# Optimization experiments

Hardware: AMD Instinct MI355X
Metric: run time of the kernel (lower is better)

The kernel has to match this reference:

```python
import jax, jax.numpy as jnp
import numpy as np

N = 11616          # IMDB total nodes (hard-coded slices in source)
NHID = 512
L = 4              # num_layers (encoder and decoder each)
E = 371712         # ~32 avg degree
SIZES = [4278, 2081, 5257]
FEATS = [3066, 2081, 5257]
GAMMA = 3.0


def setup_inputs() -> dict:
    key = jax.random.key(0)
    ks = jax.random.split(key, 24)
    s = 0.02
    d = {}
    d["X0"] = jax.random.normal(ks[0], (SIZES[0], FEATS[0]), jnp.float32)
    d["X1"] = jax.random.normal(ks[1], (SIZES[1], FEATS[1]), jnp.float32)
    d["X2"] = jax.random.normal(ks[2], (SIZES[2], FEATS[2]), jnp.float32)
    d["src"] = jax.random.randint(ks[3], (E,), 0, N)
    d["dst"] = jax.random.randint(ks[4], (E,), 0, N)
    d["edge_w"] = jax.random.uniform(ks[5], (E,), jnp.float32) / 32.0  # ~normalized adjacency values
    d["adj_full"] = (jax.random.uniform(ks[6], (N, N), jnp.float32) < 0.005).astype(jnp.float32)
    # input projections fc_list: feat_dim -> nhid
    for i in range(3):
        d[f"fc_W{i}"] = jax.random.normal(ks[7 + i], (FEATS[i], NHID), jnp.float32) * s
        d[f"fc_b{i}"] = jnp.zeros((NHID,), jnp.float32)
    # stacked GraphConvolution weights (encoder / decoder)
    d["enc_W"] = jax.random.normal(ks[10], (L, NHID, NHID), jnp.float32) * s
    d["enc_b"] = jnp.zeros((L, NHID), jnp.float32)
    d["dec_W"] = jax.random.normal(ks[11], (L, NHID, NHID), jnp.float32) * s
    d["dec_b"] = jnp.zeros((L, NHID), jnp.float32)
    # output projections fc_list2: nhid -> feat_dim
    for i in range(3):
        d[f"out_W{i}"] = jax.random.normal(ks[12 + i], (NHID, FEATS[i]), jnp.float32) * s
        d[f"out_b{i}"] = jnp.zeros((FEATS[i],), jnp.float32)
    return d


def reference(X0, X1, X2, edge_w, adj_full,
              fc_W0, fc_b0, fc_W1, fc_b1, fc_W2, fc_b2,
              enc_W, enc_b, dec_W, dec_b,
              out_W0, out_b0, out_W1, out_b1, out_W2, out_b2,
              src, dst):
    def spmm(h):  # sparse A @ h via edge list
        return jax.ops.segment_sum(h[src] * edge_w[:, None], dst, num_segments=N)

    # per-type input projection, concat over node types -> [N, NHID]
    x = jnp.concatenate([X0 @ fc_W0 + fc_b0,
                         X1 @ fc_W1 + fc_b1,
                         X2 @ fc_W2 + fc_b2], axis=0)

    # encoder then decoder; per source: relu+dropout only at layer 0 (L>1 branch),
    # residual add for layers i>0; dropout is identity in eval mode.
    for W, b in ((enc_W, enc_b), (dec_W, dec_b)):
        for i in range(L):
            h = spmm(x @ W[i]) + b[i]
            x = jax.nn.relu(h) if i == 0 else x + h

    # IMDB slices of final embedding
    e0, e1, e2 = x[:SIZES[0]], x[SIZES[0]:SIZES[0] + SIZES[1]], x[SIZES[0] + SIZES[1]:]
    r0 = e0 @ out_W0 + out_b0
    r1 = e1 @ out_W1 + out_b1
    r2 = e2 @ out_W2 + out_b2

    # emb_loss_fun2: BCE(sigmoid(x x^T), adj_full), mean. Stable form:
    z = x @ x.T  # [N, N]
    emb_loss = jnp.mean(adj_full * jax.nn.softplus(-z) + (1.0 - adj_full) * jax.nn.softplus(z))

    # recon_loss_fun2 on type-0 features (cosine-based, power gamma)
    rn = r0 / jnp.maximum(jnp.linalg.norm(r0, axis=-1, keepdims=True), 1e-12)
    fn = X0 / jnp.maximum(jnp.linalg.norm(X0, axis=1, keepdims=True), 1e-12)
    recon_loss = jnp.mean((1.0 - jnp.sum(rn * fn, axis=-1)) ** GAMMA)

    return (r0, r1, r2, emb_loss, recon_loss)
```

## Files before the change

### kernel.cpp

```cpp
#include <hip/hip_runtime.h>
#include <math.h>

#define N_NODES 11616
#define NROWPAD 11776
#define NHID    512
#define EDGES   371712
#define S0 4278
#define S1 2081
#define S2 5257
#define F0 3066
#define F1 2081
#define F2 5257
#define NBLK 91
#define NZBLK 4186
#define FC_KS 4
#define WPR 363

typedef __attribute__((ext_vector_type(8))) short bf16x8;
typedef __attribute__((ext_vector_type(4))) float f32x4;

#define GL2LDS(g, l) __builtin_amdgcn_global_load_lds(                         \
    (const __attribute__((address_space(1))) unsigned int*)(g),                \
    (__attribute__((address_space(3))) unsigned int*)(l), 16, 0, 0)

__device__ __forceinline__ int slot_of(int row, int kg)
{
    return row * 4 + (kg ^ ((row >> 1) & 3));
}

__device__ __forceinline__ float bf2f(short s)
{
    return __uint_as_float(((unsigned)(unsigned short)s) << 16);
}

__global__ void k_init(double* __restrict__ accum, int* __restrict__ indeg,
                       int* __restrict__ cursor)
{
    int i = blockIdx.x * blockDim.x + threadIdx.x;
    if (i < 2) accum[i] = 0.0;
    if (i < N_NODES) { indeg[i] = 0; cursor[i] = 0; }
}

__global__ void k_padzero(short* __restrict__ xh, short* __restrict__ xl)
{
    int i = blockIdx.x * blockDim.x + threadIdx.x;
    const int base  = N_NODES * NHID;
    const int total = (NROWPAD - N_NODES) * NHID;
    if (i < total) { xh[base + i] = 0; xl[base + i] = 0; }
}

__global__ void k_adjbits(const float* __restrict__ adj, unsigned* __restrict__ bits)
{
    const long i = (long)blockIdx.x * 256 + threadIdx.x;
    const long total = (long)N_NODES * WPR;
    if (i >= total) return;
    const int r = (int)(i / WPR);
    const int w = (int)(i % WPR);
    const float4* rp = reinterpret_cast<const float4*>(adj + (long)r * N_NODES + w * 32);
    unsigned m = 0;
    #pragma unroll
    for (int j4 = 0; j4 < 8; ++j4) {
        float4 v = rp[j4];
        int b = j4 * 4;
        m |= (v.x != 0.f) ? (1u << b)       : 0u;
        m |= (v.y != 0.f) ? (1u << (b + 1)) : 0u;
        m |= (v.z != 0.f) ? (1u << (b + 2)) : 0u;
        m |= (v.w != 0.f) ? (1u << (b + 3)) : 0u;
    }
    bits[i] = m;
}

__global__ void k_count(const int* __restrict__ dst, int* __restrict__ indeg)
{
    int e = blockIdx.x * blockDim.x + threadIdx.x;
    if (e < EDGES) atomicAdd(&indeg[dst[e]], 1);
}

__global__ void k_scan(const int* __restrict__ indeg, int* __restrict__ rowptr)
{
    __shared__ int part[256];
    const int t = threadIdx.x;
    const int chunk = (N_NODES + 255) / 256;
    const int base = t * chunk;
    int s = 0;
    for (int i = 0; i < chunk; ++i) {
        int idx = base + i;
        if (idx < N_NODES) s += indeg[idx];
    }
    part[t] = s;
    __syncthreads();
    if (t == 0) for (int i = 1; i < 256; ++i) part[i] += part[i - 1];
    __syncthreads();
    int run = (t == 0) ? 0 : part[t - 1];
    for (int i = 0; i < chunk; ++i) {
        int idx = base + i;
        if (idx < N_NODES) { rowptr[idx] = run; run += indeg[idx]; }
    }
    if (t == 0) rowptr[N_NODES] = part[255];
}

__global__ void k_fill(const int* __restrict__ src, const int* __restrict__ dst,
                       const float* __restrict__ ew, const int* __restrict__ rowptr,
                       int* __restrict__ cursor, int* __restrict__ csrc,
                       float* __restrict__ cw)
{
    int e = blockIdx.x * blockDim.x + threadIdx.x;
    if (e >= EDGES) return;
    int d = dst[e];
    int pos = rowptr[d] + atomicAdd(&cursor[d], 1);
    csrc[pos] = src[e];
    cw[pos]   = ew[e];
}

__device__ __forceinline__ void split_bf16(float f, short& hi, short& lo)
{
    unsigned u  = __float_as_uint(f);
    unsigned hr = (u + 0x7FFFu + ((u >> 16) & 1u)) & 0xFFFF0000u;
    float    fh = __uint_as_float(hr);
    float    fl = f - fh;
    unsigned ul = __float_as_uint(fl);
    unsigned lr = ul + 0x7FFFu + ((ul >> 16) & 1u);
    hi = (short)(hr >> 16);
    lo = (short)(lr >> 16);
}

__global__ void k_splitpad(const float* __restrict__ in, short* __restrict__ oh,
                           short* __restrict__ ol, int R, int C, int Cpad)
{
    const int c = blockIdx.x * 256 + threadIdx.x;
    const int r = blockIdx.y;
    if (c >= Cpad) return;
    float f = (r < R && c < C) ? in[(long)r * C + c] : 0.f;
    short h, l;
    split_bf16(f, h, l);
    oh[(long)r * Cpad + c] = h;
    ol[(long)r * Cpad + c] = l;
}

__global__ void k_tsplit(const float* __restrict__ in, short* __restrict__ oh,
                         short* __restrict__ ol, int R, int C, int Rpad, int Cpad)
{
    __shared__ float tile[32][33];
    const int cb = blockIdx.x * 32, rb = blockIdx.y * 32;
    const int tx = threadIdx.x, ty = threadIdx.y;
    #pragma unroll
    for (int i = ty; i < 32; i += 8) {
        int r = rb + i, c = cb + tx;
        tile[i][tx] = (r < R && c < C) ? in[(long)r * C + c] : 0.f;
    }
    __syncthreads();
    #pragma unroll
    for (int i = ty; i < 32; i += 8) {
        int row = cb + i, col = rb + tx;
        if (row < Cpad && col < Rpad) {
            short h, l;
            split_bf16(tile[tx][i], h, l);
            oh[(long)row * Rpad + col] = h;
            ol[(long)row * Rpad + col] = l;
        }
    }
}

__device__ __forceinline__ void stage_gl(const short* __restrict__ src, int ldk,
                                         int k0, short* ldsPanel, int lane)
{
    #pragma unroll
    for (int i = 0; i < 8; ++i) {
        int ci  = i * 64 + lane;
        int row = ci >> 2;
        int kgs = (ci & 3) ^ ((row >> 1) & 3);
        const short* g = src + (long)row * ldk + k0 + kgs * 8;
        GL2LDS(g, (char*)ldsPanel + i * 1024);
    }
}

__global__ __launch_bounds__(256, 3)
void k_gemm_bb(const short* __restrict__ Agh, const short* __restrict__ Agl,
               const short* __restrict__ Bgh, const short* __restrict__ Bgl,
               const float* __restrict__ bias, float* __restrict__ C,
               int M, int NN, int Kpad, int ldk)
{
    __shared__ short P[4][4096];
    const int t = threadIdx.x, lane = t & 63, w = t >> 6;
    const int rowBase = blockIdx.y * 128, colBase = blockIdx.x * 128;
    const int wm = (w >> 1) * 64, wn = (w & 1) * 64;
    const int kg = lane >> 4, fr = lane & 15;

    const short* srcs[4] = { Agh + (long)rowBase * ldk, Agl + (long)rowBase * ldk,
                             Bgh + (long)colBase * ldk, Bgl + (long)colBase * ldk };
    const short* mySrc = srcs[w];

    int offA[4], offB[4];
    #pragma unroll
    for (int f = 0; f < 4; ++f) {
        int rA = wm + f * 16 + fr, rB = wn + f * 16 + fr;
        offA[f] = slot_of(rA, kg) * 8;
        offB[f] = slot_of(rB, kg) * 8;
    }

    f32x4 acc[4][4];
    #pragma unroll
    for (int i = 0; i < 4; ++i)
        #pragma unroll
        for (int j = 0; j < 4; ++j)
            acc[i][j] = (f32x4){0.f, 0.f, 0.f, 0.f};

    for (int k0 = 0; k0 < Kpad; k0 += 32) {
        stage_gl(mySrc, ldk, k0, &P[w][0], lane);
        __syncthreads();
        bf16x8 ah[4], al[4], bh[4], bl[4];
        #pragma unroll
        for (int f = 0; f < 4; ++f) {
            ah[f] = *(const bf16x8*)&P[0][offA[f]];
            al[f] = *(const bf16x8*)&P[1][offA[f]];
            bh[f] = *(const bf16x8*)&P[2][offB[f]];
            bl[f] = *(const bf16x8*)&P[3][offB[f]];
        }
        #pragma unroll
        for (int i = 0; i < 4; ++i)
            #pragma unroll
            for (int j = 0; j < 4; ++j) {
                acc[i][j] = __builtin_amdgcn_mfma_f32_16x16x32_bf16(ah[i], bh[j], acc[i][j], 0, 0, 0);
                acc[i][j] = __builtin_amdgcn_mfma_f32_16x16x32_bf16(ah[i], bl[j], acc[i][j], 0, 0, 0);
                acc[i][j] = __builtin_amdgcn_mfma_f32_16x16x32_bf16(al[i], bh[j], acc[i][j], 0, 0, 0);
            }
        __syncthreads();
    }

    #pragma unroll
    for (int i = 0; i < 4; ++i) {
        #pragma unroll
        for (int q = 0; q < 4; ++q) {
            int r = rowBase + wm + i * 16 + kg * 4 + q;
            if (r >= M) continue;
            #pragma unroll
            for (int j = 0; j < 4; ++j) {
                int c = colBase + wn + j * 16 + fr;
                if (c < NN)
                    C[(long)r * NN + c] = acc[i][j][q] + (bias ? bias[c] : 0.f);
            }
        }
    }
}

__global__ __launch_bounds__(256, 3)
void k_gemm_red(const short* __restrict__ Agh, const short* __restrict__ Agl,
                const short* __restrict__ Bgh, const short* __restrict__ Bgl,
                float* __restrict__ Cpart, int M, int ldk, int kChunk)
{
    __shared__ short P[4][4096];
    const int t = threadIdx.x, lane = t & 63, w = t >> 6;
    const int rowBase = blockIdx.y * 128, colBase = blockIdx.x * 128;
    const int z = blockIdx.z;
    const int wm = (w >> 1) * 64, wn = (w & 1) * 64;
    const int kg = lane >> 4, fr = lane & 15;

    const short* srcs[4] = { Agh + (long)rowBase * ldk, Agl + (long)rowBase * ldk,
                             Bgh + (long)colBase * ldk, Bgl + (long)colBase * ldk };
    const short* mySrc = srcs[w];

    int offA[4], offB[4];
    #pragma unroll
    for (int f = 0; f < 4; ++f) {
        int rA = wm + f * 16 + fr, rB = wn + f * 16 + fr;
        offA[f] = slot_of(rA, kg) * 8;
        offB[f] = slot_of(rB, kg) * 8;
    }

    f32x4 acc[4][4];
    #pragma unroll
    for (int i = 0; i < 4; ++i)
        #pragma unroll
        for (int j = 0; j < 4; ++j)
            acc[i][j] = (f32x4){0.f, 0.f, 0.f, 0.f};

    const int kEnd = z * kChunk + kChunk;
    for (int k0 = z * kChunk; k0 < kEnd; k0 += 32) {
        stage_gl(mySrc, ldk, k0, &P[w][0], lane);
        __syncthreads();
        bf16x8 ah[4], al[4], bh[4], bl[4];
        #pragma unroll
        for (int f = 0; f < 4; ++f) {
            ah[f] = *(const bf16x8*)&P[0][offA[f]];
            al[f] = *(const bf16x8*)&P[1][offA[f]];
            bh[f] = *(const bf16x8*)&P[2][offB[f]];
            bl[f] = *(const bf16x8*)&P[3][offB[f]];
        }
        #pragma unroll
        for (int i = 0; i < 4; ++i)
            #pragma unroll
            for (int j = 0; j < 4; ++j) {
                acc[i][j] = __builtin_amdgcn_mfma_f32_16x16x32_bf16(ah[i], bh[j], acc[i][j], 0, 0, 0);
                acc[i][j] = __builtin_amdgcn_mfma_f32_16x16x32_bf16(ah[i], bl[j], acc[i][j], 0, 0, 0);
                acc[i][j] = __builtin_amdgcn_mfma_f32_16x16x32_bf16(al[i], bh[j], acc[i][j], 0, 0, 0);
            }
        __syncthreads();
    }

    #pragma unroll
    for (int i = 0; i < 4; ++i) {
        #pragma unroll
        for (int q = 0; q < 4; ++q) {
            int r = rowBase + wm + i * 16 + kg * 4 + q;
            if (r >= M) continue;
            #pragma unroll
            for (int j = 0; j < 4; ++j) {
                int c = colBase + wn + j * 16 + fr;
                Cpart[((long)z * M + r) * NHID + c] = acc[i][j][q];
            }
        }
    }
}

__global__ void k_fcreduce(const float* __restrict__ Cpart, const float* __restrict__ bias,
                           int M, short* __restrict__ oh, short* __restrict__ ol)
{
    const int r = blockIdx.x;
    const int c = threadIdx.x << 2;
    float4 s = *reinterpret_cast<const float4*>(bias + c);
    #pragma unroll
    for (int z = 0; z < FC_KS; ++z) {
        const float4 p = *reinterpret_cast<const float4*>(Cpart + ((long)z * M + r) * NHID + c);
        s.x += p.x; s.y += p.y; s.z += p.z; s.w += p.w;
    }
    short4 h, l;
    split_bf16(s.x, h.x, l.x); split_bf16(s.y, h.y, l.y);
    split_bf16(s.z, h.z, l.z); split_bf16(s.w, h.w, l.w);
    *reinterpret_cast<short4*>(oh + (long)r * NHID + c) = h;
    *reinterpret_cast<short4*>(ol + (long)r * NHID + c) = l;
}

__global__ __launch_bounds__(256, 3)
void k_zloss(const short* __restrict__ xh, const short* __restrict__ xl,
             const unsigned* __restrict__ bits, double* __restrict__ accum)
{
    __shared__ short P[4][4096];
    __shared__ float ztr[4][16][17];
    __shared__ float red[256];
    const int t = threadIdx.x, lane = t & 63, w = t >> 6;

    int L;
    {
        const int q = NZBLK / 8, rr = NZBLK % 8;
        int d = blockIdx.x;
        int xcd = d & 7, pos = d >> 3;
        L = (xcd < rr) ? xcd * (q + 1) + pos : rr * (q + 1) + (xcd - rr) * q + pos;
    }
    int R, Cb;
    {
        int RS = 0;
        for (;;) {
            int nr  = min(4, NBLK - RS * 4);
            int tri = nr * (nr + 1) / 2;
            int rest = NBLK - (RS + 1) * 4;
            if (rest < 0) rest = 0;
            int band = tri + nr * rest;
            if (L < band) break;
            L -= band; ++RS;
        }
        int nr  = min(4, NBLK - RS * 4);
        int tri = nr * (nr + 1) / 2;
        if (L < tri) {
            int r = 0;
            while (L >= nr - r) { L -= nr - r; ++r; }
            R  = RS * 4 + r;
            Cb = RS * 4 + r + L;
        } else {
            L -= tri;
            int CS = RS + 1;
            for (;;) {
                int nc  = min(4, NBLK - CS * 4);
                int cnt = nr * nc;
                if (L < cnt) { R = RS * 4 + L / nc; Cb = CS * 4 + L % nc; break; }
                L -= cnt; ++CS;
            }
        }
    }
    const int rowBase = R * 128, colBase = Cb * 128;
    const int diag = (Cb == R);

    const int wm = (w >> 1) * 64, wn = (w & 1) * 64;
    const int kg = lane >> 4, fr = lane & 15;

    const short* srcs[4] = { xh + (long)rowBase * NHID, xl + (long)rowBase * NHID,
                             xh + (long)colBase * NHID, xl + (long)colBase * NHID };
    const short* mySrc = srcs[w];

    int offA[4], offB[4];
    #pragma unroll
    for (int f = 0; f < 4; ++f) {
        int rA = wm + f * 16 + fr, rB = wn + f * 16 + fr;
        offA[f] = slot_of(rA, kg) * 8;
        offB[f] = slot_of(rB, kg) * 8;
    }

    f32x4 acc[4][4];
    #pragma unroll
    for (int i = 0; i < 4; ++i)
        #pragma unroll
        for (int j = 0; j < 4; ++j)
            acc[i][j] = (f32x4){0.f, 0.f, 0.f, 0.f};

    for (int k0 = 0; k0 < NHID; k0 += 32) {
        stage_gl(mySrc, NHID, k0, &P[w][0], lane);
        __syncthreads();
        bf16x8 ah[4], al[4], bh[4], bl[4];
        #pragma unroll
        for (int f = 0; f < 4; ++f) {
            ah[f] = *(const bf16x8*)&P[0][offA[f]];
            al[f] = *(const bf16x8*)&P[1][offA[f]];
            bh[f] = *(const bf16x8*)&P[2][offB[f]];
            bl[f] = *(const bf16x8*)&P[3][offB[f]];
        }
        #pragma unroll
        for (int i = 0; i < 4; ++i)
            #pragma unroll
            for (int j = 0; j < 4; ++j) {
                acc[i][j] = __builtin_amdgcn_mfma_f32_16x16x32_bf16(ah[i], bh[j], acc[i][j], 0, 0, 0);
                acc[i][j] = __builtin_amdgcn_mfma_f32_16x16x32_bf16(ah[i], bl[j], acc[i][j], 0, 0, 0);
                acc[i][j] = __builtin_amdgcn_mfma_f32_16x16x32_bf16(al[i], bh[j], acc[i][j], 0, 0, 0);
            }
        __syncthreads();
    }

    float local = 0.f;
    #pragma unroll
    for (int i = 0; i < 4; ++i) {
        #pragma unroll
        for (int q = 0; q < 4; ++q) {
            int r = rowBase + wm + i * 16 + kg * 4 + q;
            if (r >= N_NODES) continue;
            #pragma unroll
            for (int j = 0; j < 4; ++j) {
                int c = colBase + wn + j * 16 + fr;
                if (c >= N_NODES) continue;
                float z  = acc[i][j][q];
                float sp = fmaxf(z, 0.f) + __logf(1.f + __expf(-fabsf(z)));
                unsigned wd = bits[(long)r * WPR + (c >> 5)];
                float az = ((wd >> (c & 31)) & 1u) ? z : 0.f;
                local += diag ? (sp - az) : (2.f * sp - az);
            }
        }
    }
    if (!diag) {
        #pragma unroll
        for (int i = 0; i < 4; ++i) {
            #pragma unroll
            for (int j = 0; j < 4; ++j) {
                #pragma unroll
                for (int q = 0; q < 4; ++q)
                    ztr[w][kg * 4 + q][fr] = acc[i][j][q];
                #pragma unroll
                for (int q = 0; q < 4; ++q) {
                    float zt = ztr[w][fr][kg * 4 + q];
                    int cc = colBase + wn + j * 16 + kg * 4 + q;
                    int rr = rowBase + wm + i * 16 + fr;
                    if (cc < N_NODES && rr < N_NODES) {
                        unsigned wd = bits[(long)cc * WPR + (rr >> 5)];
                        if ((wd >> (rr & 31)) & 1u) local -= zt;
                    }
                }
            }
        }
    }
    red[t] = local;
    __syncthreads();
    for (int sft = 128; sft > 0; sft >>= 1) {
        if (t < sft) red[t] += red[t + sft];
        __syncthreads();
    }
    if (t == 0) atomicAdd(accum, (double)red[0]);
}

__global__ void k_spmm(const float* __restrict__ y,
                       const int* __restrict__ rowptr, const int* __restrict__ csrc,
                       const float* __restrict__ cw, const float* __restrict__ bias,
                       int do_relu, short* __restrict__ xh, short* __restrict__ xl)
{
    const int wv   = threadIdx.x >> 6;
    const int lane = threadIdx.x & 63;
    const int n    = blockIdx.x * 2 + (wv >> 1);
    const int c    = (wv & 1) * 256 + (lane << 2);
    float4 s = make_float4(0.f, 0.f, 0.f, 0.f);
    const int beg = rowptr[n], end = rowptr[n + 1];
    for (int e = beg; e < end; ++e) {
        int   sn = csrc[e];
        float wt = cw[e];
        const float4 yv = *reinterpret_cast<const float4*>(y + (long)sn * NHID + c);
        s.x = fmaf(wt, yv.x, s.x);
        s.y = fmaf(wt, yv.y, s.y);
        s.z = fmaf(wt, yv.z, s.z);
        s.w = fmaf(wt, yv.w, s.w);
    }
    const float4 bv = *reinterpret_cast<const float4*>(bias + c);
    float4 o;
    o.x = s.x + bv.x; o.y = s.y + bv.y; o.z = s.z + bv.z; o.w = s.w + bv.w;
    if (do_relu) {
        o.x = fmaxf(o.x, 0.f); o.y = fmaxf(o.y, 0.f);
        o.z = fmaxf(o.z, 0.f); o.w = fmaxf(o.w, 0.f);
    } else {
        const short4 h4 = *reinterpret_cast<const short4*>(xh + (long)n * NHID + c);
        const short4 l4 = *reinterpret_cast<const short4*>(xl + (long)n * NHID + c);
        o.x += bf2f(h4.x) + bf2f(l4.x);
        o.y += bf2f(h4.y) + bf2f(l4.y);
        o.z += bf2f(h4.z) + bf2f(l4.z);
        o.w += bf2f(h4.w) + bf2f(l4.w);
    }
    short4 h, l;
    split_bf16(o.x, h.x, l.x); split_bf16(o.y, h.y, l.y);
    split_bf16(o.z, h.z, l.z); split_bf16(o.w, h.w, l.w);
    *reinterpret_cast<short4*>(xh + (long)n * NHID + c) = h;
    *reinterpret_cast<short4*>(xl + (long)n * NHID + c) = l;
}

__global__ void k_recon(const float* __restrict__ r0, const float* __restrict__ X0,
                        double* __restrict__ accum)
{
    const int row = blockIdx.x;
    const int t = threadIdx.x;
    float dot = 0.f, nr = 0.f, nf = 0.f;
    for (int c = t; c < F0; c += 256) {
        float a = r0[(long)row * F0 + c];
        float b = X0[(long)row * F0 + c];
        dot = fmaf(a, b, dot);
        nr  = fmaf(a, a, nr);
        nf  = fmaf(b, b, nf);
    }
    #pragma unroll
    for (int o = 32; o > 0; o >>= 1) {
        dot += __shfl_down(dot, o);
        nr  += __shfl_down(nr, o);
        nf  += __shfl_down(nf, o);
    }
    __shared__ float sd[3][4];
    const int lane = t & 63, wid = t >> 6;
    if (lane == 0) { sd[0][wid] = dot; sd[1][wid] = nr; sd[2][wid] = nf; }
    __syncthreads();
    if (t == 0) {
        float d = sd[0][0] + sd[0][1] + sd[0][2] + sd[0][3];
        float a = sd[1][0] + sd[1][1] + sd[1][2] + sd[1][3];
        float b = sd[2][0] + sd[2][1] + sd[2][2] + sd[2][3];
        float cosv = d / (fmaxf(sqrtf(a), 1e-12f) * fmaxf(sqrtf(b), 1e-12f));
        float v = 1.f - cosv;
        atomicAdd(accum + 1, (double)(v * v * v));
    }
}

__global__ void k_final(const double* __restrict__ accum, float* __restrict__ out)
{
    if (threadIdx.x == 0) {
        out[45082958] = (float)(accum[0] / ((double)N_NODES * (double)N_NODES));
        out[45082959] = (float)(accum[1] / (double)S0);
    }
}

extern "C" void kernel_launch(void* const* d_in, const int* in_sizes, int n_in,
                              void* d_out, int out_size, void* d_ws, size_t ws_size,
                              hipStream_t stream)
{
    const float* X0  = (const float*)d_in[0];
    const float* X1  = (const float*)d_in[1];
    const float* X2  = (const float*)d_in[2];
    const int*   src = (const int*)d_in[3];
    const int*   dst = (const int*)d_in[4];
    const float* ew  = (const float*)d_in[5];
    const float* adj = (const float*)d_in[6];
    const float* fcW[3]  = {(const float*)d_in[7],  (const float*)d_in[9],  (const float*)d_in[11]};
    const float* fcB[3]  = {(const float*)d_in[8],  (const float*)d_in[10], (const float*)d_in[12]};
    const float* encW = (const float*)d_in[13];
    const float* encB = (const float*)d_in[14];
    const float* decW = (const float*)d_in[15];
    const float* decB = (const float*)d_in[16];
    const float* outW[3] = {(const float*)d_in[17], (const float*)d_in[19], (const float*)d_in[21]};
    const float* outB[3] = {(const float*)d_in[18], (const float*)d_in[20], (const float*)d_in[22]};
    float* out = (float*)d_out;

    const int FD[3]     = {F0, F1, F2};
    const int FPAD[3]   = {(F0 + 127) & ~127, (F1 + 127) & ~127, (F2 + 127) & ~127};
    const int SPAD[3]   = {(S0 + 127) & ~127, (S1 + 127) & ~127, (S2 + 127) & ~127};
    const int SD[3]     = {S0, S1, S2};
    const float* XD[3]  = {X0, X1, X2};

    char* ws = (char*)d_ws;
    size_t off = 0;
    auto alloc = [&](size_t bytes) { void* p = ws + off; off += (bytes + 255) & ~(size_t)255; return p; };

    double* accum = (double*)alloc(16);
    const size_t XB = (size_t)N_NODES * NHID * sizeof(float);
    float* ybuf = (float*)alloc(XB);
    float* xalt = (float*)alloc(XB);
    short* xh   = (short*)alloc((size_t)NROWPAD * NHID * 2);
    short* xl   = (short*)alloc((size_t)NROWPAD * NHID * 2);
    const size_t XSmax = (size_t)5376 * 5376;
    short* Xsh  = (short*)alloc(XSmax * 2);
    short* Xsl  = (short*)alloc(XSmax * 2);
    short* fcWh = (short*)alloc((size_t)NHID * 5376 * 2);
    short* fcWl = (short*)alloc((size_t)NHID * 5376 * 2);
    short* wTh  = (short*)alloc((size_t)8 * NHID * NHID * 2);
    short* wTl  = (short*)alloc((size_t)8 * NHID * NHID * 2);
    unsigned* bits = (unsigned*)alloc((size_t)N_NODES * WPR * 4);
    int* indeg  = (int*)alloc((size_t)N_NODES * 4);
    int* rowptr = (int*)alloc((size_t)(N_NODES + 1) * 4);
    int* cursor = (int*)alloc((size_t)N_NODES * 4);
    int* csrc   = (int*)alloc((size_t)EDGES * 4);
    float* cw   = (float*)alloc((size_t)EDGES * 4);

    float* cpart = ybuf;

    k_init<<<dim3((N_NODES + 255) / 256), dim3(256), 0, stream>>>(accum, indeg, cursor);
    k_padzero<<<dim3(((NROWPAD - N_NODES) * NHID + 255) / 256), dim3(256), 0, stream>>>(xh, xl);
    k_count<<<dim3((EDGES + 255) / 256), dim3(256), 0, stream>>>(dst, indeg);
    k_scan<<<dim3(1), dim3(256), 0, stream>>>(indeg, rowptr);
    k_fill<<<dim3((EDGES + 255) / 256), dim3(256), 0, stream>>>(src, dst, ew, rowptr, cursor, csrc, cw);
    {
        long words = (long)N_NODES * WPR;
        k_adjbits<<<dim3((unsigned)((words + 255) / 256)), dim3(256), 0, stream>>>(adj, bits);
    }

    auto tgrid = [](int Cpad, int Rpad) { return dim3((unsigned)((Cpad + 31) / 32), (unsigned)((Rpad + 31) / 32)); };
    auto ggrid = [](int m, int nn) { return dim3((unsigned)((nn + 127) / 128), (unsigned)((m + 127) / 128)); };

    for (int i = 0; i < 4; ++i) {
        k_tsplit<<<tgrid(NHID, NHID), dim3(32, 8), 0, stream>>>(
            encW + (size_t)i * NHID * NHID, wTh + (size_t)i * NHID * NHID,
            wTl + (size_t)i * NHID * NHID, NHID, NHID, NHID, NHID);
        k_tsplit<<<tgrid(NHID, NHID), dim3(32, 8), 0, stream>>>(
            decW + (size_t)i * NHID * NHID, wTh + (size_t)(4 + i) * NHID * NHID,
            wTl + (size_t)(4 + i) * NHID * NHID, NHID, NHID, NHID, NHID);
    }

    {
        size_t rowoff = 0;
        for (int i = 0; i < 3; ++i) {
            k_splitpad<<<dim3((FPAD[i] + 255) / 256, SPAD[i]), dim3(256), 0, stream>>>(
                XD[i], Xsh, Xsl, SD[i], FD[i], FPAD[i]);
            k_tsplit<<<tgrid(NHID, FPAD[i]), dim3(32, 8), 0, stream>>>(
                fcW[i], fcWh, fcWl, FD[i], NHID, FPAD[i], NHID);
            k_gemm_red<<<dim3(NHID / 128, SPAD[i] / 128, FC_KS), dim3(256), 0, stream>>>(
                Xsh, Xsl, fcWh, fcWl, cpart, SD[i], FPAD[i], FPAD[i] / FC_KS);
            k_fcreduce<<<dim3(SD[i]), dim3(128), 0, stream>>>(
                cpart, fcB[i], SD[i], xh + rowoff * NHID, xl + rowoff * NHID);
            rowoff += SD[i];
        }
    }

    for (int phase = 0; phase < 2; ++phase) {
        const float* B = phase ? decB : encB;
        for (int i = 0; i < 4; ++i) {
            k_gemm_bb<<<ggrid(N_NODES, NHID), dim3(256), 0, stream>>>(
                xh, xl, wTh + (size_t)(phase * 4 + i) * NHID * NHID,
                wTl + (size_t)(phase * 4 + i) * NHID * NHID,
                nullptr, ybuf, N_NODES, NHID, NHID, NHID);
            k_spmm<<<dim3(N_NODES / 2), dim3(256), 0, stream>>>(
                ybuf, rowptr, csrc, cw, B + (size_t)i * NHID, (i == 0) ? 1 : 0,
                xh, xl);
        }
    }

    short* oWh = Xsh;
    short* oWl = Xsl;
    {
        short *ph = oWh, *pl = oWl;
        for (int i = 0; i < 3; ++i) {
            int FDP = (FD[i] + 127) & ~127;
            k_tsplit<<<tgrid(FDP, NHID), dim3(32, 8), 0, stream>>>(
                outW[i], ph, pl, NHID, FD[i], NHID, FDP);
            ph += (size_t)FDP * NHID; pl += (size_t)FDP * NHID;
        }
    }

    {
        short *ph = oWh, *pl = oWl;
        float* oo = out;
        size_t rowoff = 0;
        for (int i = 0; i < 3; ++i) {
            int FDP = (FD[i] + 127) & ~127;
            k_gemm_bb<<<ggrid(SD[i], FD[i]), dim3(256), 0, stream>>>(
                xh + rowoff * NHID, xl + rowoff * NHID, ph, pl, outB[i], oo,
                SD[i], FD[i], NHID, NHID);
            ph += (size_t)FDP * NHID; pl += (size_t)FDP * NHID;
            oo += (size_t)SD[i] * FD[i];
            rowoff += SD[i];
        }
    }

    k_zloss<<<dim3(NZBLK), dim3(256), 0, stream>>>(xh, xl, bits, accum);
    k_recon<<<dim3(S0), dim3(256), 0, stream>>>(out, X0, accum);
    k_final<<<dim3(1), dim3(64), 0, stream>>>(accum, out);
}
```

Measured before the change: 2.254 ms.

## Enlarge output-GEMM and BCE-loss tiles to 256x256 with 512-thread blocks

Adds a 256x256-tile GEMM kernel with 8 waves for the three output projections. The x·xᵀ BCE loss kernel moves to the same 256x256 tiles, which lets its upper-triangular tile enumeration collapse to a simple loop. Larger tiles raise the ratio of MFMA work to LDS and global loads and cut the number of triangle tiles. In exchange each thread holds 128 accumulator floats, which risks register pressure or spills and lowers occupancy. More edge tiles are also partly empty, and the output weights are padded to 256 columns.

```diff
diff --git a/kernel.cpp b/kernel.cpp
--- a/kernel.cpp
+++ b/kernel.cpp
@@ -11,8 +11,8 @@
 #define F0 3066
 #define F1 2081
 #define F2 5257
-#define NBLK 91
-#define NZBLK 4186
+#define NB2 46
+#define NZB2 1081
 #define FC_KS 4
 #define WPR 363
 
@@ -174,6 +174,19 @@
     }
 }
 
+__device__ __forceinline__ void stage_gl256(const short* __restrict__ src, int ldk,
+                                            int k0, short* ldsPanel, int half, int lane)
+{
+    #pragma unroll
+    for (int i = 0; i < 8; ++i) {
+        int ci  = i * 128 + half * 64 + lane;
+        int row = ci >> 2;
+        int kgs = (ci & 3) ^ ((row >> 1) & 3);
+        const short* g = src + (long)row * ldk + k0 + kgs * 8;
+        GL2LDS(g, (char*)ldsPanel + i * 2048 + half * 1024);
+    }
+}
+
 __global__ __launch_bounds__(256, 3)
 void k_gemm_bb(const short* __restrict__ Agh, const short* __restrict__ Agl,
                const short* __restrict__ Bgh, const short* __restrict__ Bgl,
@@ -238,6 +251,75 @@
                 int c = colBase + wn + j * 16 + fr;
                 if (c < NN)
                     C[(long)r * NN + c] = acc[i][j][q] + (bias ? bias[c] : 0.f);
+            }
+        }
+    }
+}
+
+__global__ __launch_bounds__(512, 2)
+void k_gemm_bb2(const short* __restrict__ Agh, const short* __restrict__ Agl,
+                const short* __restrict__ Bgh, const short* __restrict__ Bgl,
+                const float* __restrict__ bias, float* __restrict__ C,
+                int M, int NN, int Kpad, int ldk)
+{
+    __shared__ short P[4][8192];
+    const int t = threadIdx.x, lane = t & 63, w = t >> 6;
+    const int rowBase = blockIdx.y * 256, colBase = blockIdx.x * 256;
+    const int kg = lane >> 4, fr = lane & 15;
+    const int half = w & 1;
+    const int wr = w >> 2, wc = w & 3;
+
+    const short* srcs[4] = { Agh + (long)rowBase * ldk, Agl + (long)rowBase * ldk,
+                             Bgh + (long)colBase * ldk, Bgl + (long)colBase * ldk };
+    const short* mySrc = srcs[w >> 1];
+
+    int offA[8], offB[4];
+    #pragma unroll
+    for (int i = 0; i < 8; ++i) offA[i] = slot_of(wr * 128 + i * 16 + fr, kg) * 8;
+    #pragma unroll
+    for (int j = 0; j < 4; ++j) offB[j] = slot_of(wc * 64 + j * 16 + fr, kg) * 8;
+
+    f32x4 acc[8][4];
+    #pragma unroll
+    for (int i = 0; i < 8; ++i)
+        #pragma unroll
+        for (int j = 0; j < 4; ++j)
+            acc[i][j] = (f32x4){0.f, 0.f, 0.f, 0.f};
+
+    for (int k0 = 0; k0 < Kpad; k0 += 32) {
+        stage_gl256(mySrc, ldk, k0, &P[w >> 1][0], half, lane);
+        __syncthreads();
+        bf16x8 bh[4], bl[4];
+        #pragma unroll
+        for (int j = 0; j < 4; ++j) {
+            bh[j] = *(const bf16x8*)&P[2][offB[j]];
+            bl[j] = *(const bf16x8*)&P[3][offB[j]];
+        }
+        #pragma unroll
+        for (int i = 0; i < 8; ++i) {
+            bf16x8 ah = *(const bf16x8*)&P[0][offA[i]];
+            bf16x8 al = *(const bf16x8*)&P[1][offA[i]];
+            #pragma unroll
+            for (int j = 0; j < 4; ++j) {
+                acc[i][j] = __builtin_amdgcn_mfma_f32_16x16x32_bf16(ah, bh[j], acc[i][j], 0, 0, 0);
+                acc[i][j] = __builtin_amdgcn_mfma_f32_16x16x32_bf16(ah, bl[j], acc[i][j], 0, 0, 0);
+                acc[i][j] = __builtin_amdgcn_mfma_f32_16x16x32_bf16(al, bh[j], acc[i][j], 0, 0, 0);
+            }
+        }
+        __syncthreads();
+    }
+
+    #pragma unroll
+    for (int i = 0; i < 8; ++i) {
+        #pragma unroll
+        for (int q = 0; q < 4; ++q) {
+            int r = rowBase + wr * 128 + i * 16 + kg * 4 + q;
+            if (r >= M) continue;
+            #pragma unroll
+            for (int j = 0; j < 4; ++j) {
+                int c = colBase + wc * 64 + j * 16 + fr;
+                if (c < NN)
+                    C[(long)r * NN + c] = acc[i][j][q] + bias[c];
             }
         }
     }
@@ -330,109 +412,81 @@
     *reinterpret_cast<short4*>(ol + (long)r * NHID + c) = l;
 }
 
-__global__ __launch_bounds__(256, 3)
+__global__ __launch_bounds__(512, 2)
 void k_zloss(const short* __restrict__ xh, const short* __restrict__ xl,
              const unsigned* __restrict__ bits, double* __restrict__ accum)
 {
-    __shared__ short P[4][4096];
-    __shared__ float ztr[4][16][17];
-    __shared__ float red[256];
+    __shared__ short P[4][8192];
+    __shared__ float ztr[8][16][17];
+    __shared__ float red[512];
     const int t = threadIdx.x, lane = t & 63, w = t >> 6;
 
     int L;
     {
-        const int q = NZBLK / 8, rr = NZBLK % 8;
-        int d = blockIdx.x;
-        int xcd = d & 7, pos = d >> 3;
+        const int q = NZB2 / 8, rr = NZB2 % 8;
+        int xcd = blockIdx.x & 7, pos = blockIdx.x >> 3;
         L = (xcd < rr) ? xcd * (q + 1) + pos : rr * (q + 1) + (xcd - rr) * q + pos;
     }
-    int R, Cb;
-    {
-        int RS = 0;
-        for (;;) {
-            int nr  = min(4, NBLK - RS * 4);
-            int tri = nr * (nr + 1) / 2;
-            int rest = NBLK - (RS + 1) * 4;
-            if (rest < 0) rest = 0;
-            int band = tri + nr * rest;
-            if (L < band) break;
-            L -= band; ++RS;
-        }
-        int nr  = min(4, NBLK - RS * 4);
-        int tri = nr * (nr + 1) / 2;
-        if (L < tri) {
-            int r = 0;
-            while (L >= nr - r) { L -= nr - r; ++r; }
-            R  = RS * 4 + r;
-            Cb = RS * 4 + r + L;
-        } else {
-            L -= tri;
-            int CS = RS + 1;
-            for (;;) {
-                int nc  = min(4, NBLK - CS * 4);
-                int cnt = nr * nc;
-                if (L < cnt) { R = RS * 4 + L / nc; Cb = CS * 4 + L % nc; break; }
-                L -= cnt; ++CS;
-            }
-        }
-    }
-    const int rowBase = R * 128, colBase = Cb * 128;
+    int R = 0;
+    while (L >= NB2 - R) { L -= NB2 - R; ++R; }
+    const int Cb = R + L;
+    const int rowBase = R * 256, colBase = Cb * 256;
     const int diag = (Cb == R);
 
-    const int wm = (w >> 1) * 64, wn = (w & 1) * 64;
     const int kg = lane >> 4, fr = lane & 15;
+    const int half = w & 1;
+    const int wr = w >> 2, wc = w & 3;
 
     const short* srcs[4] = { xh + (long)rowBase * NHID, xl + (long)rowBase * NHID,
                              xh + (long)colBase * NHID, xl + (long)colBase * NHID };
-    const short* mySrc = srcs[w];
-
-    int offA[4], offB[4];
-    #pragma unroll
-    for (int f = 0; f < 4; ++f) {
-        int rA = wm + f * 16 + fr, rB = wn + f * 16 + fr;
-        offA[f] = slot_of(rA, kg) * 8;
-        offB[f] = slot_of(rB, kg) * 8;
-    }
-
-    f32x4 acc[4][4];
-    #pragma unroll
-    for (int i = 0; i < 4; ++i)
+    const short* mySrc = srcs[w >> 1];
+
+    int offA[8], offB[4];
+    #pragma unroll
+    for (int i = 0; i < 8; ++i) offA[i] = slot_of(wr * 128 + i * 16 + fr, kg) * 8;
+    #pragma unroll
+    for (int j = 0; j < 4; ++j) offB[j] = slot_of(wc * 64 + j * 16 + fr, kg) * 8;
+
+    f32x4 acc[8][4];
+    #pragma unroll
+    for (int i = 0; i < 8; ++i)
         #pragma unroll
         for (int j = 0; j < 4; ++j)
             acc[i][j] = (f32x4){0.f, 0.f, 0.f, 0.f};
 
     for (int k0 = 0; k0 < NHID; k0 += 32) {
-        stage_gl(mySrc, NHID, k0, &P[w][0], lane);
-        __syncthreads();
-        bf16x8 ah[4], al[4], bh[4], bl[4];
-        #pragma unroll
-        for (int f = 0; f < 4; ++f) {
-            ah[f] = *(const bf16x8*)&P[0][offA[f]];
-            al[f] = *(const bf16x8*)&P[1][offA[f]];
-            bh[f] = *(const bf16x8*)&P[2][offB[f]];
-            bl[f] = *(const bf16x8*)&P[3][offB[f]];
-        }
-        #pragma unroll
-        for (int i = 0; i < 4; ++i)
-            #pragma unroll
-            for (int j = 0; j < 4; ++j) {
-                acc[i][j] = __builtin_amdgcn_mfma_f32_16x16x32_bf16(ah[i], bh[j], acc[i][j], 0, 0, 0);
-                acc[i][j] = __builtin_amdgcn_mfma_f32_16x16x32_bf16(ah[i], bl[j], acc[i][j], 0, 0, 0);
-                acc[i][j] = __builtin_amdgcn_mfma_f32_16x16x32_bf16(al[i], bh[j], acc[i][j], 0, 0, 0);
-            }
+        stage_gl256(mySrc, NHID, k0, &P[w >> 1][0], half, lane);
+        __syncthreads();
+        bf16x8 bh[4], bl[4];
+        #pragma unroll
+        for (int j = 0; j < 4; ++j) {
+            bh[j] = *(const bf16x8*)&P[2][offB[j]];
+            bl[j] = *(const bf16x8*)&P[3][offB[j]];
+        }
+        #pragma unroll
+        for (int i = 0; i < 8; ++i) {
+            bf16x8 ah = *(const bf16x8*)&P[0][offA[i]];
+            bf16x8 al = *(const bf16x8*)&P[1][offA[i]];
+            #pragma unroll
+            for (int j = 0; j < 4; ++j) {
+                acc[i][j] = __builtin_amdgcn_mfma_f32_16x16x32_bf16(ah, bh[j], acc[i][j], 0, 0, 0);
+                acc[i][j] = __builtin_amdgcn_mfma_f32_16x16x32_bf16(ah, bl[j], acc[i][j], 0, 0, 0);
+                acc[i][j] = __builtin_amdgcn_mfma_f32_16x16x32_bf16(al, bh[j], acc[i][j], 0, 0, 0);
+            }
+        }
         __syncthreads();
     }
 
     float local = 0.f;
     #pragma unroll
-    for (int i = 0; i < 4; ++i) {
+    for (int i = 0; i < 8; ++i) {
         #pragma unroll
         for (int q = 0; q < 4; ++q) {
-            int r = rowBase + wm + i * 16 + kg * 4 + q;
+            int r = rowBase + wr * 128 + i * 16 + kg * 4 + q;
             if (r >= N_NODES) continue;
             #pragma unroll
             for (int j = 0; j < 4; ++j) {
-                int c = colBase + wn + j * 16 + fr;
+                int c = colBase + wc * 64 + j * 16 + fr;
                 if (c >= N_NODES) continue;
                 float z  = acc[i][j][q];
                 float sp = fmaxf(z, 0.f) + __logf(1.f + __expf(-fabsf(z)));
@@ -444,7 +498,7 @@
     }
     if (!diag) {
         #pragma unroll
-        for (int i = 0; i < 4; ++i) {
+        for (int i = 0; i < 8; ++i) {
             #pragma unroll
             for (int j = 0; j < 4; ++j) {
                 #pragma unroll
@@ -453,8 +507,8 @@
                 #pragma unroll
                 for (int q = 0; q < 4; ++q) {
                     float zt = ztr[w][fr][kg * 4 + q];
-                    int cc = colBase + wn + j * 16 + kg * 4 + q;
-                    int rr = rowBase + wm + i * 16 + fr;
+                    int cc = colBase + wc * 64 + j * 16 + kg * 4 + q;
+                    int rr = rowBase + wr * 128 + i * 16 + fr;
                     if (cc < N_NODES && rr < N_NODES) {
                         unsigned wd = bits[(long)cc * WPR + (rr >> 5)];
                         if ((wd >> (rr & 31)) & 1u) local -= zt;
@@ -465,7 +519,7 @@
     }
     red[t] = local;
     __syncthreads();
-    for (int sft = 128; sft > 0; sft >>= 1) {
+    for (int sft = 256; sft > 0; sft >>= 1) {
         if (t < sft) red[t] += red[t + sft];
         __syncthreads();
     }
@@ -578,6 +632,7 @@
     const int FD[3]     = {F0, F1, F2};
     const int FPAD[3]   = {(F0 + 127) & ~127, (F1 + 127) & ~127, (F2 + 127) & ~127};
     const int SPAD[3]   = {(S0 + 127) & ~127, (S1 + 127) & ~127, (S2 + 127) & ~127};
+    const int FDP2[3]   = {(F0 + 255) & ~255, (F1 + 255) & ~255, (F2 + 255) & ~255};
     const int SD[3]     = {S0, S1, S2};
     const float* XD[3]  = {X0, X1, X2};
 
@@ -619,6 +674,7 @@
 
     auto tgrid = [](int Cpad, int Rpad) { return dim3((unsigned)((Cpad + 31) / 32), (unsigned)((Rpad + 31) / 32)); };
     auto ggrid = [](int m, int nn) { return dim3((unsigned)((nn + 127) / 128), (unsigned)((m + 127) / 128)); };
+    auto ggrid2 = [](int m, int nn) { return dim3((unsigned)((nn + 255) / 256), (unsigned)((m + 255) / 256)); };
 
     for (int i = 0; i < 4; ++i) {
         k_tsplit<<<tgrid(NHID, NHID), dim3(32, 8), 0, stream>>>(
@@ -662,10 +718,9 @@
     {
         short *ph = oWh, *pl = oWl;
         for (int i = 0; i < 3; ++i) {
-            int FDP = (FD[i] + 127) & ~127;
-            k_tsplit<<<tgrid(FDP, NHID), dim3(32, 8), 0, stream>>>(
-                outW[i], ph, pl, NHID, FD[i], NHID, FDP);
-            ph += (size_t)FDP * NHID; pl += (size_t)FDP * NHID;
+            k_tsplit<<<tgrid(FDP2[i], NHID), dim3(32, 8), 0, stream>>>(
+                outW[i], ph, pl, NHID, FD[i], NHID, FDP2[i]);
+            ph += (size_t)FDP2[i] * NHID; pl += (size_t)FDP2[i] * NHID;
         }
     }
 
@@ -674,17 +729,16 @@
         float* oo = out;
         size_t rowoff = 0;
         for (int i = 0; i < 3; ++i) {
-            int FDP = (FD[i] + 127) & ~127;
-            k_gemm_bb<<<ggrid(SD[i], FD[i]), dim3(256), 0, stream>>>(
+            k_gemm_bb2<<<ggrid2(SD[i], FD[i]), dim3(512), 0, stream>>>(
                 xh + rowoff * NHID, xl + rowoff * NHID, ph, pl, outB[i], oo,
                 SD[i], FD[i], NHID, NHID);
-            ph += (size_t)FDP * NHID; pl += (size_t)FDP * NHID;
+            ph += (size_t)FDP2[i] * NHID; pl += (size_t)FDP2[i] * NHID;
             oo += (size_t)SD[i] * FD[i];
             rowoff += SD[i];
         }
     }
 
-    k_zloss<<<dim3(NZBLK), dim3(256), 0, stream>>>(xh, xl, bits, accum);
+    k_zloss<<<dim3(NZB2), dim3(512), 0, stream>>>(xh, xl, bits, accum);
     k_recon<<<dim3(S0), dim3(256), 0, stream>>>(out, X0, accum);
     k_final<<<dim3(1), dim3(64), 0, stream>>>(accum, out);
 }
```

Measured after the change: 2.482 ms. 1.1x slower.
